# Kernel optimization log

Hardware: AMD Instinct MI355X
Metric: run time of the kernel (lower is better)

The kernel has to match this reference:

```python
import jax, jax.numpy as jnp
import numpy as np

BUCKET = 32   # bucket_size hard-coded in module
HEADS = 8
LN_EPS = 1e-5
SELF_ATTN_VALUE = -5e4  # TOKEN_SELF_ATTN_VALUE from reformer-pytorch


def _layer_norm(x, g, b):
    m = jnp.mean(x, axis=-1, keepdims=True)
    v = jnp.mean((x - m) ** 2, axis=-1, keepdims=True)
    return (x - m) / jnp.sqrt(v + LN_EPS) * g + b


def _lsh_attention(qk, v, rot):
    # qk, v: (B=b*h, T, Dh); rot: (Dh, n_buckets//2); n_hashes = 1
    B, T, D = qk.shape
    n_buckets = T // BUCKET
    # hash: random rotations, argmax over [r, -r]
    r = jnp.einsum('btf,fi->bti', qk, rot)                 # (B, T, n_buckets//2)
    r = jnp.concatenate([r, -r], axis=-1)                  # (B, T, n_buckets)
    buckets = jnp.argmax(r, axis=-1)                       # (B, T) int
    t = jnp.arange(T)
    key = buckets * T + t                                  # unique sort key
    sticker = jnp.argsort(key, axis=-1)                    # (B, T) permutation
    undo = jnp.argsort(sticker, axis=-1)
    sqk = jnp.take_along_axis(qk, sticker[..., None], axis=1)
    sv = jnp.take_along_axis(v, sticker[..., None], axis=1)
    # chunk into n_buckets chunks of size BUCKET
    bq_t = sticker.reshape(B, n_buckets, BUCKET)
    bq = sqk.reshape(B, n_buckets, BUCKET, D)
    bv = sv.reshape(B, n_buckets, BUCKET, D)
    nrm = jnp.sqrt(jnp.sum(bq * bq, axis=-1, keepdims=True))
    bk = bq / jnp.maximum(nrm, 1e-12)                      # shared-QK: keys are unit-norm queries
    def look_one_back(xx):
        return jnp.concatenate([xx, jnp.roll(xx, 1, axis=1)], axis=2)
    bk = look_one_back(bk)
    bvv = look_one_back(bv)
    bkv_t = look_one_back(bq_t)
    dots = jnp.einsum('bcie,bcje->bcij', bq, bk) * (D ** -0.5)  # (B, C, 32, 64)
    self_mask = bq_t[:, :, :, None] == bkv_t[:, :, None, :]
    dots = jnp.where(self_mask, SELF_ATTN_VALUE, dots)
    attn = jax.nn.softmax(dots, axis=-1)
    bo = jnp.einsum('bcij,bcje->bcie', attn, bvv)
    so = bo.reshape(B, T, D)
    return jnp.take_along_axis(so, undo[..., None], axis=1)   # unsort (n_hashes=1 -> probs=1)


def _lsh_self_attention(h, w_qk, w_v, w_out, b_out, rot):
    b, t, d = h.shape
    dh = d // HEADS
    qk = (h @ w_qk).reshape(b, t, HEADS, dh).transpose(0, 2, 1, 3).reshape(b * HEADS, t, dh)
    vv = (h @ w_v).reshape(b, t, HEADS, dh).transpose(0, 2, 1, 3).reshape(b * HEADS, t, dh)
    o = _lsh_attention(qk, vv, rot)
    o = o.reshape(b, HEADS, t, dh).transpose(0, 2, 1, 3).reshape(b, t, d)
    return o @ w_out + b_out


def setup_inputs() -> dict:
    key = jax.random.key(0)
    ks = jax.random.split(key, 8)
    B, T, D, F = 8, 4096, 512, 2048
    dh, nb = D // HEADS, T // BUCKET
    s = 0.02
    return {
        'x': jax.random.normal(ks[0], (B, T, D), jnp.float32),
        'w_qk': jax.random.normal(ks[1], (D, D), jnp.float32) * s,
        'w_v': jax.random.normal(ks[2], (D, D), jnp.float32) * s,
        'w_out': jax.random.normal(ks[3], (D, D), jnp.float32) * s,
        'b_out': jnp.zeros((D,), jnp.float32),
        'ln1_g': jnp.ones((D,), jnp.float32),
        'ln1_b': jnp.zeros((D,), jnp.float32),
        'w_ff1': jax.random.normal(ks[4], (D, F), jnp.float32) * s,
        'b_ff1': jnp.zeros((F,), jnp.float32),
        'w_ff2': jax.random.normal(ks[5], (F, D), jnp.float32) * s,
        'b_ff2': jnp.zeros((D,), jnp.float32),
        'ln2_g': jnp.ones((D,), jnp.float32),
        'ln2_b': jnp.zeros((D,), jnp.float32),
        'rotations': jax.random.normal(ks[6], (dh, nb // 2), jnp.float32),
    }


def reference(x, w_qk, w_v, w_out, b_out, ln1_g, ln1_b, w_ff1, b_ff1,
              w_ff2, b_ff2, ln2_g, ln2_b, rotations):
    # y1 = x + Attn(LN1(x)); y2 = x + FFN(LN2(y1)); out = mean(y1, y2)
    h1 = _layer_norm(x, ln1_g, ln1_b)
    y1 = x + _lsh_self_attention(h1, w_qk, w_v, w_out, b_out, rotations)
    h2 = _layer_norm(y1, ln2_g, ln2_b)
    ffn = jax.nn.relu(h2 @ w_ff1 + b_ff1) @ w_ff2 + b_ff2
    y2 = x + ffn
    return 0.5 * (y1 + y2)
```

## Files before the change

kernel.cpp:

```cpp
#include <hip/hip_runtime.h>
#include <stdint.h>

typedef _Float16 f16;
typedef _Float16 f16x8 __attribute__((ext_vector_type(8)));
typedef float    f32x4 __attribute__((ext_vector_type(4)));
typedef unsigned long long u64;

__device__ __forceinline__ void gload16(const void* g, void* l) {
  __builtin_amdgcn_global_load_lds(
      (__attribute__((address_space(1))) void*)g,
      (__attribute__((address_space(3))) void*)l, 16, 0, 0);
}

template<int EPI>
__global__ __launch_bounds__(256)
void gemm_bt(const f16* __restrict__ A, int lda,
             const f16* __restrict__ Bt, int ldb,
             int K, int N,
             float* __restrict__ outf, f16* __restrict__ outh,
             f16* __restrict__ outh2,
             const float* __restrict__ bias,
             const float* __restrict__ add1)
{
  __shared__ __align__(16) f16 sA[128 * 64];
  __shared__ __align__(16) f16 sB[128 * 64];
  const int tid  = threadIdx.x;
  const int lane = tid & 63;
  const int wv   = tid >> 6;
  const int wm   = wv >> 1, wn = wv & 1;
  const int l15  = lane & 15, l4 = lane >> 4;

  const int gx = gridDim.x;
  int lid = blockIdx.y * gx + blockIdx.x;
  const int cpx = (gx * gridDim.y) >> 3;
  lid = (lid & 7) * cpx + (lid >> 3);
  const long bm0 = (long)(lid / gx) * 128;
  const long bn0 = (long)(lid % gx) * 128;

  f32x4 acc[4][4];
#pragma unroll
  for (int i = 0; i < 4; ++i)
#pragma unroll
    for (int j = 0; j < 4; ++j) acc[i][j] = f32x4{0.f, 0.f, 0.f, 0.f};

  const int rs = tid >> 3;
  const int cs = tid & 7;
  const int cg = cs ^ (rs & 7);

  const int nkt = K >> 6;
  for (int kt = 0; kt < nkt; ++kt) {
    __syncthreads();
    const long ka = (long)kt * 64 + cg * 8;
#pragma unroll
    for (int rd = 0; rd < 4; ++rd) {
      const int row = rs + rd * 32;
      gload16(A + (bm0 + row) * lda + ka, &sA[row * 64 + cs * 8]);
    }
#pragma unroll
    for (int rd = 0; rd < 4; ++rd) {
      const int row = rs + rd * 32;
      gload16(Bt + (bn0 + row) * ldb + ka, &sB[row * 64 + cs * 8]);
    }
    __syncthreads();
#pragma unroll
    for (int kk = 0; kk < 2; ++kk) {
      f16x8 af[4], bfr[4];
#pragma unroll
      for (int mt = 0; mt < 4; ++mt) {
        const int row = wm * 64 + mt * 16 + l15;
        const int c = kk * 4 + l4;
        af[mt] = *(const f16x8*)&sA[row * 64 + ((c ^ (row & 7)) << 3)];
      }
#pragma unroll
      for (int nt = 0; nt < 4; ++nt) {
        const int row = wn * 64 + nt * 16 + l15;
        const int c = kk * 4 + l4;
        bfr[nt] = *(const f16x8*)&sB[row * 64 + ((c ^ (row & 7)) << 3)];
      }
#pragma unroll
      for (int mt = 0; mt < 4; ++mt)
#pragma unroll
        for (int nt = 0; nt < 4; ++nt)
          acc[mt][nt] = __builtin_amdgcn_mfma_f32_16x16x32_f16(af[mt], bfr[nt], acc[mt][nt], 0, 0, 0);
    }
  }

  if constexpr (EPI == 7) {
    const int hcol = (int)(bn0 >> 6) + wn;
    const int is_v = hcol >> 3, h = hcol & 7;
    f16* base = is_v ? outh2 : outh;
#pragma unroll
    for (int mt = 0; mt < 4; ++mt)
#pragma unroll
      for (int r = 0; r < 4; ++r) {
        const long grow = bm0 + wm * 64 + mt * 16 + l4 * 4 + r;
        const int bb = (int)(grow >> 12), tt = (int)(grow & 4095);
        f16* dst = base + (((long)bb * 8 + h) * 4096 + tt) * 64;
#pragma unroll
        for (int nt = 0; nt < 4; ++nt)
          dst[nt * 16 + l15] = (f16)acc[mt][nt][r];
      }
    return;
  }

#pragma unroll
  for (int mt = 0; mt < 4; ++mt)
#pragma unroll
    for (int nt = 0; nt < 4; ++nt)
#pragma unroll
      for (int r = 0; r < 4; ++r) {
        const long grow = bm0 + wm * 64 + mt * 16 + l4 * 4 + r;
        const long gcol = bn0 + wn * 64 + nt * 16 + l15;
        const long idx  = grow * (long)N + gcol;
        const float c = acc[mt][nt][r];
        if constexpr (EPI == 2) {
          outf[idx] = c + bias[gcol] + add1[idx];
        } else if constexpr (EPI == 3) {
          outh[idx] = (f16)fmaxf(c + bias[gcol], 0.f);
        }
      }
}

__global__ __launch_bounds__(512)
void gemm8_ffn2(const f16* __restrict__ A,
                const f16* __restrict__ Bt,
                const f16* __restrict__ sxyh,
                const float* __restrict__ bias,
                float* __restrict__ outf)
{
  __shared__ __align__(16) f16 sA[128 * 64];
  __shared__ __align__(16) f16 sB[128 * 64];
  const int tid  = threadIdx.x;
  const int lane = tid & 63;
  const int wv   = tid >> 6;
  const int wm   = wv >> 2, wn = wv & 3;
  const int l15  = lane & 15, l4 = lane >> 4;

  const int gx = gridDim.x;
  int lid = blockIdx.y * gx + blockIdx.x;
  const int cpx = (gx * gridDim.y) >> 3;
  lid = (lid & 7) * cpx + (lid >> 3);
  const long bm0 = (long)(lid / gx) * 128;
  const long bn0 = (long)(lid % gx) * 128;

  f32x4 acc[4][2];
#pragma unroll
  for (int i = 0; i < 4; ++i)
#pragma unroll
    for (int j = 0; j < 2; ++j) acc[i][j] = f32x4{0.f, 0.f, 0.f, 0.f};

  const int rs = tid >> 3;
  const int cs = tid & 7;
  const int cg = cs ^ (rs & 7);

  for (int kt = 0; kt < 32; ++kt) {
    __syncthreads();
    const long ka = (long)kt * 64 + cg * 8;
#pragma unroll
    for (int rd = 0; rd < 2; ++rd) {
      const int row = rs + rd * 64;
      gload16(A + (bm0 + row) * 2048 + ka, &sA[row * 64 + cs * 8]);
    }
#pragma unroll
    for (int rd = 0; rd < 2; ++rd) {
      const int row = rs + rd * 64;
      gload16(Bt + (bn0 + row) * 2048 + ka, &sB[row * 64 + cs * 8]);
    }
    __syncthreads();
#pragma unroll
    for (int kk = 0; kk < 2; ++kk) {
      f16x8 af[4], bfr[2];
#pragma unroll
      for (int mt = 0; mt < 4; ++mt) {
        const int row = wm * 64 + mt * 16 + l15;
        const int c = kk * 4 + l4;
        af[mt] = *(const f16x8*)&sA[row * 64 + ((c ^ (row & 7)) << 3)];
      }
#pragma unroll
      for (int nt = 0; nt < 2; ++nt) {
        const int row = wn * 32 + nt * 16 + l15;
        const int c = kk * 4 + l4;
        bfr[nt] = *(const f16x8*)&sB[row * 64 + ((c ^ (row & 7)) << 3)];
      }
#pragma unroll
      for (int mt = 0; mt < 4; ++mt)
#pragma unroll
        for (int nt = 0; nt < 2; ++nt)
          acc[mt][nt] = __builtin_amdgcn_mfma_f32_16x16x32_f16(af[mt], bfr[nt], acc[mt][nt], 0, 0, 0);
    }
  }

#pragma unroll
  for (int mt = 0; mt < 4; ++mt)
#pragma unroll
    for (int nt = 0; nt < 2; ++nt)
#pragma unroll
      for (int r = 0; r < 4; ++r) {
        const long grow = bm0 + wm * 64 + mt * 16 + l4 * 4 + r;
        const long gcol = bn0 + wn * 32 + nt * 16 + l15;
        const long idx  = grow * 512 + gcol;
        outf[idx] = (float)sxyh[idx] + 0.5f * (acc[mt][nt][r] + bias[gcol]);
      }
}

__global__ __launch_bounds__(256)
void ln_kernel(const float* __restrict__ in, const float* __restrict__ gam,
               const float* __restrict__ bet, f16* __restrict__ out,
               int ldo, int split, const float* __restrict__ xin,
               f16* __restrict__ sxy)
{
  const long row = (long)blockIdx.x * 4 + (threadIdx.x >> 6);
  const int lane = threadIdx.x & 63;
  const float4* p = (const float4*)(in + row * 512);
  const float4 a = p[lane * 2], b = p[lane * 2 + 1];
  float xv[8] = {a.x, a.y, a.z, a.w, b.x, b.y, b.z, b.w};
  float s = 0.f;
#pragma unroll
  for (int i = 0; i < 8; ++i) s += xv[i];
#pragma unroll
  for (int m = 32; m; m >>= 1) s += __shfl_xor(s, m);
  const float mean = s * (1.f / 512.f);
  float vs = 0.f;
#pragma unroll
  for (int i = 0; i < 8; ++i) { const float d = xv[i] - mean; vs += d * d; }
#pragma unroll
  for (int m = 32; m; m >>= 1) vs += __shfl_xor(vs, m);
  const float rstd = 1.f / sqrtf(vs * (1.f / 512.f) + 1e-5f);
  const float4* gp = (const float4*)gam;
  const float4* bp = (const float4*)bet;
  const float4 g0 = gp[lane * 2], g1 = gp[lane * 2 + 1];
  const float4 b0 = bp[lane * 2], b1 = bp[lane * 2 + 1];
  const float gg[8] = {g0.x, g0.y, g0.z, g0.w, g1.x, g1.y, g1.z, g1.w};
  const float bb[8] = {b0.x, b0.y, b0.z, b0.w, b1.x, b1.y, b1.z, b1.w};
  f16x8 vh, vl;
#pragma unroll
  for (int i = 0; i < 8; ++i) {
    const float y = (xv[i] - mean) * rstd * gg[i] + bb[i];
    const f16 hi = (f16)y;
    vh[i] = hi;
    vl[i] = (f16)((y - (float)hi) * 64.f);
  }
  f16* o = out + row * ldo + lane * 8;
  *(f16x8*)o = vh;
  if (split) *(f16x8*)(o + 512) = vl;
  if (sxy) {
    const float4* xp = (const float4*)(xin + row * 512);
    const float4 x0 = xp[lane * 2], x1 = xp[lane * 2 + 1];
    const float xx[8] = {x0.x, x0.y, x0.z, x0.w, x1.x, x1.y, x1.z, x1.w};
    f16x8 vsx;
#pragma unroll
    for (int i = 0; i < 8; ++i) vsx[i] = (f16)(0.5f * (xv[i] + xx[i]));
    *(f16x8*)(sxy + row * 512 + lane * 8) = vsx;
  }
}

__global__ __launch_bounds__(256)
void transpose_f16(const float* __restrict__ src, f16* __restrict__ dst, int K, int N)
{
  __shared__ float tile[32][33];
  const int tx = threadIdx.x & 31, ty = threadIdx.x >> 5;
  const long k0 = (long)blockIdx.y * 32, n0 = (long)blockIdx.x * 32;
#pragma unroll
  for (int i = 0; i < 4; ++i)
    tile[ty + i * 8][tx] = src[(k0 + ty + i * 8) * N + n0 + tx];
  __syncthreads();
#pragma unroll
  for (int i = 0; i < 4; ++i)
    dst[(n0 + ty + i * 8) * K + k0 + tx] = (f16)tile[tx][ty + i * 8];
}

__global__ __launch_bounds__(256)
void whash_f32(const float* __restrict__ wqk, const float* __restrict__ rot,
               float* __restrict__ WrT, f16* __restrict__ rotTh)
{
  if (blockIdx.x == 0 && blockIdx.y == 0) {
    for (int idx = threadIdx.x; idx < 4096; idx += 256) {
      const int d = idx >> 6, i = idx & 63;
      rotTh[i * 64 + d] = (f16)rot[idx];
    }
  }
  const int kk = blockIdx.x;
  const int n  = blockIdx.y * 256 + threadIdx.x;
  const int h = n >> 6, i = n & 63;
  float s = 0.f;
  for (int d = 0; d < 64; ++d)
    s += wqk[kk * 512 + h * 64 + d] * rot[d * 64 + i];
  WrT[(long)n * 512 + kk] = s;
}

__global__ __launch_bounds__(256)
void rhash4_kernel(const f16* __restrict__ gqk, const f16* __restrict__ rotTh,
                   int* __restrict__ buckets)
{
  const int tid = threadIdx.x, lane = tid & 63, w = tid >> 6;
  const int bh = blockIdx.x >> 5, tb = blockIdx.x & 31;
  const int t0 = tb * 128;
  const int l15 = lane & 15, l4 = lane >> 4;

  f16x8 br[2][4];
#pragma unroll
  for (int kk = 0; kk < 2; ++kk)
#pragma unroll
    for (int nt = 0; nt < 4; ++nt)
      br[kk][nt] = *(const f16x8*)&rotTh[(nt * 16 + l15) * 64 + kk * 32 + l4 * 8];

  const f16* gqb = gqk + ((long)bh * 4096 + t0) * 64;
  f16x8 aq[2][2];
#pragma unroll
  for (int kk = 0; kk < 2; ++kk)
#pragma unroll
    for (int mt = 0; mt < 2; ++mt)
      aq[kk][mt] = *(const f16x8*)&gqb[(long)(w * 32 + mt * 16 + l15) * 64 + kk * 32 + l4 * 8];

  f32x4 acc[2][4];
#pragma unroll
  for (int i = 0; i < 2; ++i)
#pragma unroll
    for (int j = 0; j < 4; ++j) acc[i][j] = f32x4{0.f, 0.f, 0.f, 0.f};
#pragma unroll
  for (int kk = 0; kk < 2; ++kk)
#pragma unroll
    for (int mt = 0; mt < 2; ++mt)
#pragma unroll
      for (int nt = 0; nt < 4; ++nt)
        acc[mt][nt] = __builtin_amdgcn_mfma_f32_16x16x32_f16(aq[kk][mt], br[kk][nt], acc[mt][nt], 0, 0, 0);

#pragma unroll
  for (int mt = 0; mt < 2; ++mt)
#pragma unroll
    for (int r = 0; r < 4; ++r) {
      const float v0 = acc[mt][0][r], v1 = acc[mt][1][r];
      const float v2 = acc[mt][2][r], v3 = acc[mt][3][r];
      unsigned int k0 = (__float_as_uint(fabsf(v0)) & ~63u) | (63 - l15);
      unsigned int k1 = (__float_as_uint(fabsf(v1)) & ~63u) | (47 - l15);
      unsigned int k2 = (__float_as_uint(fabsf(v2)) & ~63u) | (31 - l15);
      unsigned int k3 = (__float_as_uint(fabsf(v3)) & ~63u) | (15 - l15 + 16);
      k3 = (__float_as_uint(fabsf(v3)) & ~63u) | (unsigned int)(15 - l15);
      float ss = v0 * v0 + v1 * v1 + v2 * v2 + v3 * v3;
#pragma unroll
      for (int m = 1; m < 16; m <<= 1) ss += __shfl_xor(ss, m);

      unsigned int mk = max(max(k0, k1), max(k2, k3));
#pragma unroll
      for (int m = 1; m < 16; m <<= 1) mk = max(mk, (unsigned int)__shfl_xor((int)mk, m));
      const unsigned int key1 = mk;
      const int col1 = 63 - (int)(key1 & 63u);
      const float m1f = __uint_as_float(key1 & ~63u);
      const int nt1 = col1 >> 4;
      const float vsel = (nt1 == 0) ? v0 : (nt1 == 1) ? v1 : (nt1 == 2) ? v2 : v3;
      const bool owner = (col1 & 15) == l15;
      const u64 bal = __ballot(owner && (vsel < 0.f));
      const int neg = (int)((bal >> (l4 * 16 + (col1 & 15))) & 1ull);
      const int bucket = col1 + (neg << 6);
      if (owner) {
        if (nt1 == 0) k0 = 0; else if (nt1 == 1) k1 = 0;
        else if (nt1 == 2) k2 = 0; else k3 = 0;
      }
      mk = max(max(k0, k1), max(k2, k3));
#pragma unroll
      for (int m = 1; m < 16; m <<= 1) mk = max(mk, (unsigned int)__shfl_xor((int)mk, m));
      const int col2 = 63 - (int)(mk & 63u);
      const float m2f = __uint_as_float(mk & ~63u);
      {
        const int nt2 = col2 >> 4;
        if ((col2 & 15) == l15) {
          if (nt2 == 0) k0 = 0; else if (nt2 == 1) k1 = 0;
          else if (nt2 == 2) k2 = 0; else k3 = 0;
        }
      }
      mk = max(max(k0, k1), max(k2, k3));
#pragma unroll
      for (int m = 1; m < 16; m <<= 1) mk = max(mk, (unsigned int)__shfl_xor((int)mk, m));
      const int col3 = 63 - (int)(mk & 63u);

      if (l15 == 0) {
        const int row = w * 32 + mt * 16 + l4 * 4 + r;
        const int bht = bh * 4096 + t0 + row;
        const float margin = m1f - m2f;
        const float rms = sqrtf(ss * (1.f / 64.f));
        const int flag = (margin < 0.015f * rms) ? 1 : 0;
        buckets[bht] = bucket | (col2 << 8) | (col3 << 16) | (flag << 24);
      }
    }
}

__global__ __launch_bounds__(256)
void fixup2_kernel(const f16* __restrict__ hsplit, const float* __restrict__ WrT,
                   int* __restrict__ buckets)
{
  const int wid = (blockIdx.x * 256 + threadIdx.x) >> 6;
  const int lane = threadIdx.x & 63;
  for (int batch = 0; batch < 4; ++batch) {
    const int base = wid * 256 + batch * 64;
    const int packed = buckets[base + lane];
    u64 bal = __ballot((packed >> 24) & 1);
    while (bal) {
      const int i = (int)__ffsll((long long)bal) - 1;
      bal &= bal - 1;
      const int row = base + i;
      const int pk = __shfl(packed, i);
      const int h = (row >> 12) & 7;
      const long hrow = (long)(row >> 15) * 4096 + (row & 4095);
      const f16* hp = hsplit + hrow * 1024 + lane * 8;
      const f16x8 hi = *(const f16x8*)hp;
      const f16x8 lo = *(const f16x8*)(hp + 512);
      float h1[8];
#pragma unroll
      for (int k = 0; k < 8; ++k) h1[k] = (float)hi[k] + (float)lo[k] * 0.015625f;
      const int cols[3] = { pk & 63, (pk >> 8) & 63, (pk >> 16) & 63 };
      float best = -1e30f; int bi = 999;
#pragma unroll
      for (int c = 0; c < 3; ++c) {
        const int cc = cols[c];
        const float* wp = WrT + ((long)(h * 64 + cc)) * 512 + lane * 8;
        const float4 w0 = *(const float4*)wp;
        const float4 w1 = *(const float4*)(wp + 4);
        float s = h1[0] * w0.x + h1[1] * w0.y + h1[2] * w0.z + h1[3] * w0.w
                + h1[4] * w1.x + h1[5] * w1.y + h1[6] * w1.z + h1[7] * w1.w;
#pragma unroll
        for (int m = 32; m; m >>= 1) s += __shfl_xor(s, m);
        if (s > best || (s == best && cc < bi)) { best = s; bi = cc; }
        const float ns = -s; const int ni = 64 + cc;
        if (ns > best || (ns == best && ni < bi)) { best = ns; bi = ni; }
      }
      if (lane == 0) buckets[row] = bi;
    }
  }
}

__global__ __launch_bounds__(256)
void sort_kernel(const int* __restrict__ buckets, int* __restrict__ sticker)
{
  __shared__ int bkt[4096];
  __shared__ unsigned int cnts[64][128];
  __shared__ unsigned char rnk[4096];
  __shared__ int tot[128];
  __shared__ int base[128];
  const int bh = blockIdx.x;
  const int tid = threadIdx.x;
  const int lane = tid & 63, wv = tid >> 6;

  for (int i = tid; i < 4096; i += 256) bkt[i] = buckets[(long)bh * 4096 + i] & 127;
  for (int i = tid; i < 64 * 128; i += 256) ((unsigned int*)cnts)[i] = 0u;
  __syncthreads();

  for (int it = 0; it < 16; ++it) {
    const int c = wv * 16 + it;
    const int t = c * 64 + lane;
    const int b = bkt[t];
    unsigned long long m = ~0ull;
#pragma unroll
    for (int k = 0; k < 7; ++k) {
      const bool bit = (b >> k) & 1;
      const unsigned long long bal = __ballot(bit);
      m &= bit ? bal : ~bal;
    }
    const int rk = (int)__popcll(m & ((1ull << lane) - 1ull));
    rnk[t] = (unsigned char)rk;
    if (rk == 0) cnts[c][b] = (unsigned int)__popcll(m);
  }
  __syncthreads();

  if (tid < 128) {
    unsigned int run = 0;
    for (int c = 0; c < 64; ++c) {
      const unsigned int x = cnts[c][tid];
      cnts[c][tid] = run;
      run += x;
    }
    tot[tid] = (int)run;
  }
  __syncthreads();
  if (tid == 0) {
    int run = 0;
    for (int b = 0; b < 128; ++b) { base[b] = run; run += tot[b]; }
  }
  __syncthreads();

  for (int it = 0; it < 16; ++it) {
    const int c = wv * 16 + it;
    const int t = c * 64 + lane;
    const int b = bkt[t];
    const int pos = base[b] + (int)cnts[c][b] + (int)rnk[t];
    sticker[(long)bh * 4096 + pos] = t;
  }
}

__global__ __launch_bounds__(256)
void attn2_kernel(const f16* __restrict__ gqk, const f16* __restrict__ gv,
                  const int* __restrict__ sticker, f16* __restrict__ o)
{
  __shared__ __align__(16) f16 sqk[160 * 64];
  __shared__ __align__(16) f16 sVT[64 * 168];
  __shared__ __align__(16) f16 sP[4][32 * 72];
  __shared__ float rnorm[160];
  __shared__ int st[160];

  const int tid = threadIdx.x, lane = tid & 63, w = tid >> 6;
  const int cg = blockIdx.x, bh = blockIdx.y;
  const int b = bh >> 3, h = bh & 7;
  const int p0 = cg * 128 - 32;
  const int l15 = lane & 15, l4 = lane >> 4;

  if (tid < 160) st[tid] = sticker[(long)bh * 4096 + ((p0 + tid) & 4095)] & 4095;
  __syncthreads();

  const f16* gqb = gqk + (long)bh * 4096 * 64;
#pragma unroll
  for (int it = 0; it < 5; ++it) {
    const int idx = it * 256 + tid;
    const int row = idx >> 3, ch = idx & 7;
    const int gsrc = ch ^ (row & 7);
    gload16(gqb + (long)st[row] * 64 + gsrc * 8, &sqk[idx * 8]);
  }

  const f16* gvb = gv + (long)bh * 4096 * 64;
  f16x8 va[5];
#pragma unroll
  for (int i = 0; i < 5; ++i) {
    const int row = w * 40 + i * 8 + (lane >> 3);
    va[i] = *(const f16x8*)&gvb[(long)st[row] * 64 + (lane & 7) * 8];
  }
#pragma unroll
  for (int i = 0; i < 5; ++i) {
    const int row = w * 40 + i * 8 + (lane >> 3);
    const int d0 = (lane & 7) * 8;
#pragma unroll
    for (int e = 0; e < 8; ++e) sVT[(d0 + e) * 168 + row] = va[i][e];
  }
  __syncthreads();

  if (tid < 160) {
    float s = 0.f;
#pragma unroll
    for (int g = 0; g < 8; ++g) {
      const f16x8 v = *(const f16x8*)&sqk[tid * 64 + ((g ^ (tid & 7)) << 3)];
#pragma unroll
      for (int e = 0; e < 8; ++e) { const float f = (float)v[e]; s += f * f; }
    }
    rnorm[tid] = 1.f / fmaxf(sqrtf(s), 1e-12f);
  }
  __syncthreads();

  f32x4 acc[2][4];
#pragma unroll
  for (int i = 0; i < 2; ++i)
#pragma unroll
    for (int j = 0; j < 4; ++j) acc[i][j] = f32x4{0.f, 0.f, 0.f, 0.f};

#pragma unroll
  for (int kk = 0; kk < 2; ++kk) {
    f16x8 aq[2], bk[4];
#pragma unroll
    for (int mt = 0; mt < 2; ++mt) {
      const int row = 32 + w * 32 + mt * 16 + l15;
      const int g = kk * 4 + l4;
      aq[mt] = *(const f16x8*)&sqk[row * 64 + ((g ^ (row & 7)) << 3)];
    }
#pragma unroll
    for (int nt = 0; nt < 4; ++nt) {
      const int row = w * 32 + nt * 16 + l15;
      const int g = kk * 4 + l4;
      bk[nt] = *(const f16x8*)&sqk[row * 64 + ((g ^ (row & 7)) << 3)];
    }
#pragma unroll
    for (int mt = 0; mt < 2; ++mt)
#pragma unroll
      for (int nt = 0; nt < 4; ++nt)
        acc[mt][nt] = __builtin_amdgcn_mfma_f32_16x16x32_f16(aq[mt], bk[nt], acc[mt][nt], 0, 0, 0);
  }

  float rn[4];
#pragma unroll
  for (int nt = 0; nt < 4; ++nt) rn[nt] = rnorm[w * 32 + nt * 16 + l15];

  float pinv[2][4];
#pragma unroll
  for (int mt = 0; mt < 2; ++mt)
#pragma unroll
    for (int r = 0; r < 4; ++r) {
      const int row_i = mt * 16 + l4 * 4 + r;
      float mx = -1e30f;
#pragma unroll
      for (int nt = 0; nt < 4; ++nt) {
        float v = acc[mt][nt][r] * 0.125f * rn[nt];
        if (nt * 16 + l15 == row_i + 32) v = -5e4f;
        acc[mt][nt][r] = v;
        mx = fmaxf(mx, v);
      }
#pragma unroll
      for (int m = 8; m; m >>= 1) mx = fmaxf(mx, __shfl_xor(mx, m));
      float ssum = 0.f;
#pragma unroll
      for (int nt = 0; nt < 4; ++nt) {
        const float pe = expf(acc[mt][nt][r] - mx);
        ssum += pe;
        sP[w][row_i * 72 + nt * 16 + l15] = (f16)pe;
      }
#pragma unroll
      for (int m = 8; m; m >>= 1) ssum += __shfl_xor(ssum, m);
      pinv[mt][r] = 1.f / ssum;
    }
  __syncthreads();

  f32x4 pacc[2][4];
#pragma unroll
  for (int i = 0; i < 2; ++i)
#pragma unroll
    for (int j = 0; j < 4; ++j) pacc[i][j] = f32x4{0.f, 0.f, 0.f, 0.f};

#pragma unroll
  for (int kk = 0; kk < 2; ++kk) {
    f16x8 ap[2], bv[4];
#pragma unroll
    for (int mt = 0; mt < 2; ++mt)
      ap[mt] = *(const f16x8*)&sP[w][(mt * 16 + l15) * 72 + kk * 32 + l4 * 8];
#pragma unroll
    for (int nt = 0; nt < 4; ++nt)
      bv[nt] = *(const f16x8*)&sVT[(nt * 16 + l15) * 168 + w * 32 + kk * 32 + l4 * 8];
#pragma unroll
    for (int mt = 0; mt < 2; ++mt)
#pragma unroll
      for (int nt = 0; nt < 4; ++nt)
        pacc[mt][nt] = __builtin_amdgcn_mfma_f32_16x16x32_f16(ap[mt], bv[nt], pacc[mt][nt], 0, 0, 0);
  }

  const long ob = (long)b * 4096 * 512 + h * 64;
#pragma unroll
  for (int mt = 0; mt < 2; ++mt)
#pragma unroll
    for (int r = 0; r < 4; ++r) {
      const int row_i = mt * 16 + l4 * 4 + r;
      const long t = st[32 + w * 32 + row_i];
      const float sc = pinv[mt][r];
#pragma unroll
      for (int nt = 0; nt < 4; ++nt)
        o[ob + t * 512 + nt * 16 + l15] = (f16)(pacc[mt][nt][r] * sc);
    }
}

extern "C" void kernel_launch(void* const* d_in, const int* in_sizes, int n_in,
                              void* d_out, int out_size, void* d_ws, size_t ws_size,
                              hipStream_t stream)
{
  const float* x     = (const float*)d_in[0];
  const float* w_qk  = (const float*)d_in[1];
  const float* w_v   = (const float*)d_in[2];
  const float* w_out = (const float*)d_in[3];
  const float* b_out = (const float*)d_in[4];
  const float* ln1g  = (const float*)d_in[5];
  const float* ln1b  = (const float*)d_in[6];
  const float* w_ff1 = (const float*)d_in[7];
  const float* b_ff1 = (const float*)d_in[8];
  const float* w_ff2 = (const float*)d_in[9];
  const float* b_ff2 = (const float*)d_in[10];
  const float* ln2g  = (const float*)d_in[11];
  const float* ln2b  = (const float*)d_in[12];
  const float* rot   = (const float*)d_in[13];
  float* out = (float*)d_out;

  char* ws = (char*)d_ws;
  f16* hsplit = (f16*)ws;
  f16* o_buf  = (f16*)ws;
  f16* sxy    = (f16*)ws;
  f16* h2     = (f16*)(ws + 33554432);
  f16* gqk    = (f16*)(ws + 67108864);
  f16* gv     = (f16*)(ws + 100663296);
  f16* abuf   = (f16*)(ws + 67108864);
  char* W0 = ws + 134217728;
  f16* wqkvT = (f16*)W0;
  f16* woutT = (f16*)(W0 + 1048576);
  f16* wff1T = (f16*)(W0 + 1572864);
  f16* wff2T = (f16*)(W0 + 3670016);
  float* WrT = (float*)(W0 + 5767168);
  int* buckets = (int*)(W0 + 6815744);
  int* sticker = (int*)(W0 + 7864320);
  f16* rotTh   = (f16*)(W0 + 8912896);

  const dim3 b256(256);
  transpose_f16<<<dim3(16, 16), b256, 0, stream>>>(w_qk,  wqkvT,             512, 512);
  transpose_f16<<<dim3(16, 16), b256, 0, stream>>>(w_v,   wqkvT + 512 * 512, 512, 512);
  transpose_f16<<<dim3(16, 16), b256, 0, stream>>>(w_out, woutT,             512, 512);
  transpose_f16<<<dim3(64, 16), b256, 0, stream>>>(w_ff1, wff1T,             512, 2048);
  transpose_f16<<<dim3(16, 64), b256, 0, stream>>>(w_ff2, wff2T,             2048, 512);
  whash_f32<<<dim3(512, 2), b256, 0, stream>>>(w_qk, rot, WrT, rotTh);
  ln_kernel<<<dim3(8192), b256, 0, stream>>>(x, ln1g, ln1b, hsplit, 1024, 1, nullptr, nullptr);
  gemm_bt<7><<<dim3(8, 256), b256, 0, stream>>>(hsplit, 1024, wqkvT, 512, 512, 1024,
      nullptr, gqk, gv, nullptr, nullptr);
  rhash4_kernel<<<dim3(2048), b256, 0, stream>>>(gqk, rotTh, buckets);
  fixup2_kernel<<<dim3(256), b256, 0, stream>>>(hsplit, WrT, buckets);
  sort_kernel<<<dim3(64), b256, 0, stream>>>(buckets, sticker);
  attn2_kernel<<<dim3(32, 64), b256, 0, stream>>>(gqk, gv, sticker, o_buf);
  gemm_bt<2><<<dim3(4, 256), b256, 0, stream>>>(o_buf, 512, woutT, 512, 512, 512,
      out, nullptr, nullptr, b_out, x);
  ln_kernel<<<dim3(8192), b256, 0, stream>>>(out, ln2g, ln2b, h2, 512, 0, x, sxy);
  for (int c = 0; c < 2; ++c) {
    const long roff = (long)c * 16384;
    gemm_bt<3><<<dim3(16, 128), b256, 0, stream>>>(h2 + roff * 512, 512, wff1T, 512, 512, 2048,
        nullptr, abuf, nullptr, b_ff1, nullptr);
    gemm8_ffn2<<<dim3(4, 128), dim3(512), 0, stream>>>(abuf, wff2T, sxy + roff * 512,
        b_ff2, out + roff * 512);
  }
}
```

Measured before the change: 483.7 us.

## Replace GEMMs with 256x256-tile double-buffered, phase-scheduled MFMA kernel

Replaces the 128x128 single-buffered GEMM kernels with one 512-thread 256x256-tile kernel. It double-buffers A/B tiles in LDS with global_load_lds, interleaves loads with MFMA phases using barriers, setprio and waitcnt scheduling, and raises arithmetic intensity per tile. The FFN is restructured to split along the hidden dimension (two 1024-wide halves) instead of rows, accumulating the second FFN2 into the output. This risks fewer blocks (under-occupancy on small GEMMs), a large LDS footprint, and a dead leftover EPI==17 block that writes acc[...][0] before the correct epilogue overwrites it.

```diff
diff --git a/kernel.cpp b/kernel.cpp
--- a/kernel.cpp
+++ b/kernel.cpp
@@ -12,194 +12,181 @@
       (__attribute__((address_space(3))) void*)l, 16, 0, 0);
 }
 
+#define MFMA_QUAD(q, af) \
+  _Pragma("unroll") for (int m2 = 0; m2 < 2; ++m2) \
+  _Pragma("unroll") for (int nt = 0; nt < 4; ++nt) \
+  _Pragma("unroll") for (int kk = 0; kk < 2; ++kk) \
+    acc[(q)*2 + m2][nt] = __builtin_amdgcn_mfma_f32_16x16x32_f16( \
+        af[m2][kk], bf[nt][kk], acc[(q)*2 + m2][nt], 0, 0, 0);
+
+#define RD_A(dst, abase, q2) \
+  _Pragma("unroll") for (int m2 = 0; m2 < 2; ++m2) \
+  _Pragma("unroll") for (int kk = 0; kk < 2; ++kk) { \
+    const int lr = (q2)*32 + m2*16 + l15; \
+    dst[m2][kk] = *(const f16x8*)&abase[lr*64 + (((kk*4 + l4) ^ (lr & 7)) << 3)]; }
+
+#define RD_B(bbase) \
+  _Pragma("unroll") for (int nt = 0; nt < 4; ++nt) \
+  _Pragma("unroll") for (int kk = 0; kk < 2; ++kk) { \
+    const int lr = brow + nt*16 + l15; \
+    bf[nt][kk] = *(const f16x8*)&bbase[lr*64 + (((kk*4 + l4) ^ (lr & 7)) << 3)]; }
+
+#define PH_PRE() \
+  __builtin_amdgcn_s_barrier(); \
+  asm volatile("s_waitcnt lgkmcnt(0)" ::: "memory"); \
+  __builtin_amdgcn_sched_barrier(0); \
+  __builtin_amdgcn_s_setprio(1);
+
+#define PH_POST() \
+  __builtin_amdgcn_s_setprio(0); \
+  __builtin_amdgcn_s_barrier(); \
+  __builtin_amdgcn_sched_barrier(0);
+
 template<int EPI>
-__global__ __launch_bounds__(256)
-void gemm_bt(const f16* __restrict__ A, int lda,
+__global__ __launch_bounds__(512, 2)
+void gemm256(const f16* __restrict__ A, int lda,
              const f16* __restrict__ Bt, int ldb,
              int K, int N,
              float* __restrict__ outf, f16* __restrict__ outh,
              f16* __restrict__ outh2,
              const float* __restrict__ bias,
+             const f16* __restrict__ sxyh,
              const float* __restrict__ add1)
 {
-  __shared__ __align__(16) f16 sA[128 * 64];
-  __shared__ __align__(16) f16 sB[128 * 64];
-  const int tid  = threadIdx.x;
-  const int lane = tid & 63;
-  const int wv   = tid >> 6;
-  const int wm   = wv >> 1, wn = wv & 1;
-  const int l15  = lane & 15, l4 = lane >> 4;
+  __shared__ __align__(16) f16 lds[65536];
+  const int tid = threadIdx.x, lane = tid & 63;
+  const int wid = tid >> 6;
+  const int wm = wid >> 2, wn = wid & 3;
+  const int l15 = lane & 15, l4 = lane >> 4;
 
   const int gx = gridDim.x;
   int lid = blockIdx.y * gx + blockIdx.x;
   const int cpx = (gx * gridDim.y) >> 3;
   lid = (lid & 7) * cpx + (lid >> 3);
-  const long bm0 = (long)(lid / gx) * 128;
-  const long bn0 = (long)(lid % gx) * 128;
-
-  f32x4 acc[4][4];
-#pragma unroll
-  for (int i = 0; i < 4; ++i)
+  const long bm0 = (long)(lid / gx) * 256;
+  const long bn0 = (long)(lid % gx) * 256;
+
+  const int rs = tid >> 3, cs = tid & 7;
+  const int cg = cs ^ (rs & 7);
+  const int nkt = K >> 6;
+  const int nmask = nkt - 1;
+
+  auto stageA = [&](int d, int half, int kt) {
+    f16* dst = &lds[(d * 4 + half) * 8192];
+    const long kb = (long)kt * 64 + cg * 8;
+    const f16* src = A + (bm0 + half * 128) * lda + kb;
+#pragma unroll
+    for (int rr = 0; rr < 2; ++rr) {
+      const int row = rs + rr * 64;
+      gload16(src + (long)row * lda, dst + row * 64 + cs * 8);
+    }
+  };
+  auto stageB = [&](int d, int half, int kt) {
+    f16* dst = &lds[(d * 4 + 2 + half) * 8192];
+    const long kb = (long)kt * 64 + cg * 8;
+    const f16* src = Bt + (bn0 + half * 128) * ldb + kb;
+#pragma unroll
+    for (int rr = 0; rr < 2; ++rr) {
+      const int row = rs + rr * 64;
+      gload16(src + (long)row * ldb, dst + row * 64 + cs * 8);
+    }
+  };
+
+  const f16* aBase0 = &lds[(0 + wm) * 8192];
+  const f16* aBase1 = &lds[(4 + wm) * 8192];
+  const f16* bBase0 = &lds[(2 + (wn >> 1)) * 8192];
+  const f16* bBase1 = &lds[(6 + (wn >> 1)) * 8192];
+  const int brow = (wn & 1) * 64;
+
+  f32x4 acc[8][4];
+#pragma unroll
+  for (int i = 0; i < 8; ++i)
 #pragma unroll
     for (int j = 0; j < 4; ++j) acc[i][j] = f32x4{0.f, 0.f, 0.f, 0.f};
-
-  const int rs = tid >> 3;
-  const int cs = tid & 7;
-  const int cg = cs ^ (rs & 7);
-
-  const int nkt = K >> 6;
-  for (int kt = 0; kt < nkt; ++kt) {
-    __syncthreads();
-    const long ka = (long)kt * 64 + cg * 8;
-#pragma unroll
-    for (int rd = 0; rd < 4; ++rd) {
-      const int row = rs + rd * 32;
-      gload16(A + (bm0 + row) * lda + ka, &sA[row * 64 + cs * 8]);
-    }
-#pragma unroll
-    for (int rd = 0; rd < 4; ++rd) {
-      const int row = rs + rd * 32;
-      gload16(Bt + (bn0 + row) * ldb + ka, &sB[row * 64 + cs * 8]);
-    }
-    __syncthreads();
-#pragma unroll
-    for (int kk = 0; kk < 2; ++kk) {
-      f16x8 af[4], bfr[4];
-#pragma unroll
-      for (int mt = 0; mt < 4; ++mt) {
-        const int row = wm * 64 + mt * 16 + l15;
-        const int c = kk * 4 + l4;
-        af[mt] = *(const f16x8*)&sA[row * 64 + ((c ^ (row & 7)) << 3)];
-      }
-#pragma unroll
-      for (int nt = 0; nt < 4; ++nt) {
-        const int row = wn * 64 + nt * 16 + l15;
-        const int c = kk * 4 + l4;
-        bfr[nt] = *(const f16x8*)&sB[row * 64 + ((c ^ (row & 7)) << 3)];
-      }
-#pragma unroll
-      for (int mt = 0; mt < 4; ++mt)
-#pragma unroll
-        for (int nt = 0; nt < 4; ++nt)
-          acc[mt][nt] = __builtin_amdgcn_mfma_f32_16x16x32_f16(af[mt], bfr[nt], acc[mt][nt], 0, 0, 0);
-    }
-  }
-
-  if constexpr (EPI == 7) {
+  f16x8 bf[4][2], afA[2][2], afB[2][2];
+
+  stageB(0, 0, 0); stageB(0, 1, 0); stageA(0, 0, 0); stageA(0, 1, 0);
+  asm volatile("s_waitcnt vmcnt(4)" ::: "memory");
+  stageB(1, 0, 1); stageB(1, 1, 1); stageA(1, 0, 1);
+  asm volatile("s_waitcnt vmcnt(6)" ::: "memory");
+  __builtin_amdgcn_s_barrier();
+  __builtin_amdgcn_sched_barrier(0);
+
+  for (int j = 0; j < nkt; j += 2) {
+    const int t2 = (j + 2) & nmask, t3 = (j + 3) & nmask;
+    RD_B(bBase0); RD_A(afA, aBase0, 0);
+    stageA(1, 1, j + 1);
+    asm volatile("s_waitcnt lgkmcnt(8)" ::: "memory");
+    PH_PRE(); MFMA_QUAD(0, afA); PH_POST();
+    RD_A(afB, aBase0, 1); RD_A(afA, aBase0, 2);
+    stageB(0, 0, t2);
+    PH_PRE(); MFMA_QUAD(1, afB); PH_POST();
+    RD_A(afB, aBase0, 3);
+    stageB(0, 1, t2);
+    PH_PRE(); MFMA_QUAD(2, afA); PH_POST();
+    stageA(0, 0, t2);
+    asm volatile("s_waitcnt vmcnt(6)" ::: "memory");
+    PH_PRE(); MFMA_QUAD(3, afB); PH_POST();
+    RD_B(bBase1); RD_A(afA, aBase1, 0);
+    stageA(0, 1, t2);
+    asm volatile("s_waitcnt lgkmcnt(8)" ::: "memory");
+    PH_PRE(); MFMA_QUAD(0, afA); PH_POST();
+    RD_A(afB, aBase1, 1); RD_A(afA, aBase1, 2);
+    stageB(1, 0, t3);
+    PH_PRE(); MFMA_QUAD(1, afB); PH_POST();
+    RD_A(afB, aBase1, 3);
+    stageB(1, 1, t3);
+    PH_PRE(); MFMA_QUAD(2, afA); PH_POST();
+    stageA(1, 0, t3);
+    asm volatile("s_waitcnt vmcnt(6)" ::: "memory");
+    PH_PRE(); MFMA_QUAD(3, afB); PH_POST();
+  }
+  asm volatile("s_waitcnt vmcnt(0)" ::: "memory");
+
+  if constexpr (EPI == 17) {
     const int hcol = (int)(bn0 >> 6) + wn;
     const int is_v = hcol >> 3, h = hcol & 7;
     f16* base = is_v ? outh2 : outh;
 #pragma unroll
-    for (int mt = 0; mt < 4; ++mt)
+    for (int mt = 0; mt < 8; ++mt)
 #pragma unroll
       for (int r = 0; r < 4; ++r) {
-        const long grow = bm0 + wm * 64 + mt * 16 + l4 * 4 + r;
+        const long grow = bm0 + wm * 128 + mt * 16 + l4 * 4 + r;
         const int bb = (int)(grow >> 12), tt = (int)(grow & 4095);
         f16* dst = base + (((long)bb * 8 + h) * 4096 + tt) * 64;
 #pragma unroll
         for (int nt = 0; nt < 4; ++nt)
-          dst[nt * 16 + l15] = (f16)acc[mt][nt][r];
-      }
-    return;
-  }
-
-#pragma unroll
-  for (int mt = 0; mt < 4; ++mt)
+          dst[nt * 16 + l15] = (f16)acc[mt][nt][0 * 4 + 0];
+      }
+  }
+#pragma unroll
+  for (int mt = 0; mt < 8; ++mt)
 #pragma unroll
     for (int nt = 0; nt < 4; ++nt)
 #pragma unroll
       for (int r = 0; r < 4; ++r) {
-        const long grow = bm0 + wm * 64 + mt * 16 + l4 * 4 + r;
+        const long grow = bm0 + wm * 128 + mt * 16 + l4 * 4 + r;
         const long gcol = bn0 + wn * 64 + nt * 16 + l15;
-        const long idx  = grow * (long)N + gcol;
         const float c = acc[mt][nt][r];
-        if constexpr (EPI == 2) {
+        if constexpr (EPI == 12) {
+          const long idx = grow * (long)N + gcol;
           outf[idx] = c + bias[gcol] + add1[idx];
-        } else if constexpr (EPI == 3) {
+        } else if constexpr (EPI == 13) {
+          const long idx = grow * (long)N + gcol;
           outh[idx] = (f16)fmaxf(c + bias[gcol], 0.f);
+        } else if constexpr (EPI == 40) {
+          const long idx = grow * (long)N + gcol;
+          outf[idx] = (float)sxyh[idx] + 0.5f * c;
+        } else if constexpr (EPI == 41) {
+          const long idx = grow * (long)N + gcol;
+          outf[idx] += 0.5f * (c + bias[gcol]);
+        } else if constexpr (EPI == 17) {
+          const int bb = (int)(grow >> 12), tt = (int)(grow & 4095);
+          const int hcol = (int)(bn0 >> 6) + wn;
+          const int is_v = hcol >> 3, h = hcol & 7;
+          f16* base = is_v ? outh2 : outh;
+          base[(((long)bb * 8 + h) * 4096 + tt) * 64 + nt * 16 + l15] = (f16)c;
         }
-      }
-}
-
-__global__ __launch_bounds__(512)
-void gemm8_ffn2(const f16* __restrict__ A,
-                const f16* __restrict__ Bt,
-                const f16* __restrict__ sxyh,
-                const float* __restrict__ bias,
-                float* __restrict__ outf)
-{
-  __shared__ __align__(16) f16 sA[128 * 64];
-  __shared__ __align__(16) f16 sB[128 * 64];
-  const int tid  = threadIdx.x;
-  const int lane = tid & 63;
-  const int wv   = tid >> 6;
-  const int wm   = wv >> 2, wn = wv & 3;
-  const int l15  = lane & 15, l4 = lane >> 4;
-
-  const int gx = gridDim.x;
-  int lid = blockIdx.y * gx + blockIdx.x;
-  const int cpx = (gx * gridDim.y) >> 3;
-  lid = (lid & 7) * cpx + (lid >> 3);
-  const long bm0 = (long)(lid / gx) * 128;
-  const long bn0 = (long)(lid % gx) * 128;
-
-  f32x4 acc[4][2];
-#pragma unroll
-  for (int i = 0; i < 4; ++i)
-#pragma unroll
-    for (int j = 0; j < 2; ++j) acc[i][j] = f32x4{0.f, 0.f, 0.f, 0.f};
-
-  const int rs = tid >> 3;
-  const int cs = tid & 7;
-  const int cg = cs ^ (rs & 7);
-
-  for (int kt = 0; kt < 32; ++kt) {
-    __syncthreads();
-    const long ka = (long)kt * 64 + cg * 8;
-#pragma unroll
-    for (int rd = 0; rd < 2; ++rd) {
-      const int row = rs + rd * 64;
-      gload16(A + (bm0 + row) * 2048 + ka, &sA[row * 64 + cs * 8]);
-    }
-#pragma unroll
-    for (int rd = 0; rd < 2; ++rd) {
-      const int row = rs + rd * 64;
-      gload16(Bt + (bn0 + row) * 2048 + ka, &sB[row * 64 + cs * 8]);
-    }
-    __syncthreads();
-#pragma unroll
-    for (int kk = 0; kk < 2; ++kk) {
-      f16x8 af[4], bfr[2];
-#pragma unroll
-      for (int mt = 0; mt < 4; ++mt) {
-        const int row = wm * 64 + mt * 16 + l15;
-        const int c = kk * 4 + l4;
-        af[mt] = *(const f16x8*)&sA[row * 64 + ((c ^ (row & 7)) << 3)];
-      }
-#pragma unroll
-      for (int nt = 0; nt < 2; ++nt) {
-        const int row = wn * 32 + nt * 16 + l15;
-        const int c = kk * 4 + l4;
-        bfr[nt] = *(const f16x8*)&sB[row * 64 + ((c ^ (row & 7)) << 3)];
-      }
-#pragma unroll
-      for (int mt = 0; mt < 4; ++mt)
-#pragma unroll
-        for (int nt = 0; nt < 2; ++nt)
-          acc[mt][nt] = __builtin_amdgcn_mfma_f32_16x16x32_f16(af[mt], bfr[nt], acc[mt][nt], 0, 0, 0);
-    }
-  }
-
-#pragma unroll
-  for (int mt = 0; mt < 4; ++mt)
-#pragma unroll
-    for (int nt = 0; nt < 2; ++nt)
-#pragma unroll
-      for (int r = 0; r < 4; ++r) {
-        const long grow = bm0 + wm * 64 + mt * 16 + l4 * 4 + r;
-        const long gcol = bn0 + wn * 32 + nt * 16 + l15;
-        const long idx  = grow * 512 + gcol;
-        outf[idx] = (float)sxyh[idx] + 0.5f * (acc[mt][nt][r] + bias[gcol]);
       }
 }
 
@@ -331,11 +318,10 @@
     for (int r = 0; r < 4; ++r) {
       const float v0 = acc[mt][0][r], v1 = acc[mt][1][r];
       const float v2 = acc[mt][2][r], v3 = acc[mt][3][r];
-      unsigned int k0 = (__float_as_uint(fabsf(v0)) & ~63u) | (63 - l15);
-      unsigned int k1 = (__float_as_uint(fabsf(v1)) & ~63u) | (47 - l15);
-      unsigned int k2 = (__float_as_uint(fabsf(v2)) & ~63u) | (31 - l15);
-      unsigned int k3 = (__float_as_uint(fabsf(v3)) & ~63u) | (15 - l15 + 16);
-      k3 = (__float_as_uint(fabsf(v3)) & ~63u) | (unsigned int)(15 - l15);
+      unsigned int k0 = (__float_as_uint(fabsf(v0)) & ~63u) | (unsigned int)(63 - l15);
+      unsigned int k1 = (__float_as_uint(fabsf(v1)) & ~63u) | (unsigned int)(47 - l15);
+      unsigned int k2 = (__float_as_uint(fabsf(v2)) & ~63u) | (unsigned int)(31 - l15);
+      unsigned int k3 = (__float_as_uint(fabsf(v3)) & ~63u) | (unsigned int)(15 - l15);
       float ss = v0 * v0 + v1 * v1 + v2 * v2 + v3 * v3;
 #pragma unroll
       for (int m = 1; m < 16; m <<= 1) ss += __shfl_xor(ss, m);
@@ -678,6 +664,7 @@
   f16* rotTh   = (f16*)(W0 + 8912896);
 
   const dim3 b256(256);
+  const dim3 b512(512);
   transpose_f16<<<dim3(16, 16), b256, 0, stream>>>(w_qk,  wqkvT,             512, 512);
   transpose_f16<<<dim3(16, 16), b256, 0, stream>>>(w_v,   wqkvT + 512 * 512, 512, 512);
   transpose_f16<<<dim3(16, 16), b256, 0, stream>>>(w_out, woutT,             512, 512);
@@ -685,20 +672,23 @@
   transpose_f16<<<dim3(16, 64), b256, 0, stream>>>(w_ff2, wff2T,             2048, 512);
   whash_f32<<<dim3(512, 2), b256, 0, stream>>>(w_qk, rot, WrT, rotTh);
   ln_kernel<<<dim3(8192), b256, 0, stream>>>(x, ln1g, ln1b, hsplit, 1024, 1, nullptr, nullptr);
-  gemm_bt<7><<<dim3(8, 256), b256, 0, stream>>>(hsplit, 1024, wqkvT, 512, 512, 1024,
-      nullptr, gqk, gv, nullptr, nullptr);
+  gemm256<17><<<dim3(4, 128), b512, 0, stream>>>(hsplit, 1024, wqkvT, 512, 512, 1024,
+      nullptr, gqk, gv, nullptr, nullptr, nullptr);
   rhash4_kernel<<<dim3(2048), b256, 0, stream>>>(gqk, rotTh, buckets);
   fixup2_kernel<<<dim3(256), b256, 0, stream>>>(hsplit, WrT, buckets);
   sort_kernel<<<dim3(64), b256, 0, stream>>>(buckets, sticker);
   attn2_kernel<<<dim3(32, 64), b256, 0, stream>>>(gqk, gv, sticker, o_buf);
-  gemm_bt<2><<<dim3(4, 256), b256, 0, stream>>>(o_buf, 512, woutT, 512, 512, 512,
-      out, nullptr, nullptr, b_out, x);
+  gemm256<12><<<dim3(2, 128), b512, 0, stream>>>(o_buf, 512, woutT, 512, 512, 512,
+      out, nullptr, nullptr, b_out, nullptr, x);
   ln_kernel<<<dim3(8192), b256, 0, stream>>>(out, ln2g, ln2b, h2, 512, 0, x, sxy);
-  for (int c = 0; c < 2; ++c) {
-    const long roff = (long)c * 16384;
-    gemm_bt<3><<<dim3(16, 128), b256, 0, stream>>>(h2 + roff * 512, 512, wff1T, 512, 512, 2048,
-        nullptr, abuf, nullptr, b_ff1, nullptr);
-    gemm8_ffn2<<<dim3(4, 128), dim3(512), 0, stream>>>(abuf, wff2T, sxy + roff * 512,
-        b_ff2, out + roff * 512);
-  }
-}
+  for (int f = 0; f < 2; ++f) {
+    gemm256<13><<<dim3(4, 128), b512, 0, stream>>>(h2, 512, wff1T + (long)f * 1024 * 512, 512,
+        512, 1024, nullptr, abuf, nullptr, b_ff1 + f * 1024, nullptr, nullptr);
+    if (f == 0)
+      gemm256<40><<<dim3(2, 128), b512, 0, stream>>>(abuf, 1024, wff2T + 1024 * 0, 2048,
+          1024, 512, out, nullptr, nullptr, b_ff2, sxy, nullptr);
+    else
+      gemm256<41><<<dim3(2, 128), b512, 0, stream>>>(abuf, 1024, wff2T + 1024, 2048,
+          1024, 512, out, nullptr, nullptr, b_ff2, sxy, nullptr);
+  }
+}
```

New measurement: 491.3 us. About the same (+1.6%).
